# Optimization experiments

Measured on AMD Instinct MI355X. Metric: run time of the kernel, lower is better.

Reference implementation:

```python
import jax, jax.numpy as jnp
import numpy as np

N = 500_000
D = 256  # input_dim
H = 256  # hidden_dim
CLAMP = 10.0


def setup_inputs() -> dict:
    key = jax.random.key(0)
    ks = jax.random.split(key, 7)
    inputs = jax.random.normal(ks[0], (N, D), dtype=jnp.float32)
    query = jax.random.normal(ks[1], (D,), dtype=jnp.float32)
    mask = jax.random.randint(ks[2], (N,), 0, 2, dtype=jnp.int32)
    # nn.Linear(in, out, bias=False).weight has shape (out, in); scale like torch default
    s = 1.0 / np.sqrt(D)
    W_query = jax.random.uniform(ks[3], (H, D), jnp.float32, -s, s)
    W_key = jax.random.uniform(ks[4], (H, D), jnp.float32, -s, s)
    W_value = jax.random.uniform(ks[5], (H, D), jnp.float32, -s, s)
    sh = 1.0 / np.sqrt(H)
    W_out = jax.random.uniform(ks[6], (H,), jnp.float32, -sh, sh)
    return {"inputs": inputs, "query": query, "mask": mask,
            "W_query": W_query, "W_key": W_key, "W_value": W_value, "W_out": W_out}


def reference(inputs, query, mask, W_query, W_key, W_value, W_out):
    # Q: [H], K,V: [N,H]
    Q = W_query @ query
    K = jnp.einsum('nd,hd->nh', inputs, W_key)
    V = jnp.einsum('nd,hd->nh', inputs, W_value)
    scale = jnp.sqrt(jnp.asarray(H, dtype=inputs.dtype))
    scores = (K @ Q) / scale                      # [N]
    scores = jnp.where(mask == 0, -jnp.inf, scores)
    weights = jax.nn.softmax(scores, axis=-1)     # [N]
    attended = weights[:, None] * V               # [N,H] (elementwise, no sum)
    logits = attended @ W_out                     # [N]
    return CLAMP * jnp.tanh(logits)
```

## Files before the change

### kernel.cpp

```cpp
#include <hip/hip_runtime.h>
#include <math.h>

typedef float f4 __attribute__((ext_vector_type(4)));

#define DIM 256
#define NF4 64
#define NB_MAIN 2048

__device__ inline float dot4(f4 a, f4 b) {
  return a.x * b.x + a.y * b.y + a.z * b.z + a.w * b.w;
}

__device__ inline void sm_combine(float& m, float& l, float bm, float bl) {
  float mn = fmaxf(m, bm);
  float e1 = (l  != 0.f) ? __expf(m  - mn) : 0.f;
  float e2 = (bl != 0.f) ? __expf(bm - mn) : 0.f;
  l = l * e1 + bl * e2;
  m = mn;
}

__global__ void qba_compute_Q(const float* __restrict__ Wq,
                              const float* __restrict__ query,
                              float* __restrict__ Q) {
  int lane = threadIdx.x & 63;
  int wid  = threadIdx.x >> 6;
  int h = blockIdx.x * 4 + wid;
  f4 w = reinterpret_cast<const f4*>(Wq + (size_t)h * DIM)[lane];
  f4 q = reinterpret_cast<const f4*>(query)[lane];
  float acc = dot4(w, q);
  #pragma unroll
  for (int off = 32; off > 0; off >>= 1) acc += __shfl_xor(acc, off);
  if (lane == 0) Q[h] = acc;
}

__global__ void qba_compute_eff(const float* __restrict__ Wk,
                                const float* __restrict__ Wv,
                                const float* __restrict__ Q,
                                const float* __restrict__ Wout,
                                float* __restrict__ q_eff,
                                float* __restrict__ v_eff) {
  int d = threadIdx.x;
  if (blockIdx.x == 0) {
    float a = 0.f;
    #pragma unroll 8
    for (int h = 0; h < DIM; ++h) a += Wk[(size_t)h * DIM + d] * Q[h];
    q_eff[d] = a * 0.0625f;
  } else {
    float a = 0.f;
    #pragma unroll 8
    for (int h = 0; h < DIM; ++h) a += Wv[(size_t)h * DIM + d] * Wout[h];
    v_eff[d] = a;
  }
}

__global__ void __launch_bounds__(256)
qba_main(const float* __restrict__ inputs,
         const int* __restrict__ mask,
         const float* __restrict__ q_eff,
         const float* __restrict__ v_eff,
         float* __restrict__ s_buf,
         float* __restrict__ t_buf,
         float* __restrict__ block_m,
         float* __restrict__ block_l,
         int N) {
  int lane = threadIdx.x & 63;
  int wid  = threadIdx.x >> 6;
  int g    = lane >> 4;
  int sub  = lane & 15;
  const f4* in4 = reinterpret_cast<const f4*>(inputs);

  f4 qe[4], ve[4];
  #pragma unroll
  for (int k = 0; k < 4; ++k) {
    qe[k] = reinterpret_cast<const f4*>(q_eff)[sub + 16 * k];
    ve[k] = reinterpret_cast<const f4*>(v_eff)[sub + 16 * k];
  }

  int wave   = blockIdx.x * 4 + wid;
  int stride = NB_MAIN * 4 * 4;
  float m = -INFINITY, l = 0.f;

  for (int n0 = wave * 4; n0 < N; n0 += stride) {
    int row  = n0 + g;
    int rowc = row < N ? row : N - 1;
    const f4* rp = in4 + (size_t)rowc * NF4 + sub;
    f4 x0 = __builtin_nontemporal_load(rp);
    f4 x1 = __builtin_nontemporal_load(rp + 16);
    f4 x2 = __builtin_nontemporal_load(rp + 32);
    f4 x3 = __builtin_nontemporal_load(rp + 48);
    int mk = mask[rowc];

    float s = dot4(x0, qe[0]) + dot4(x1, qe[1]) + dot4(x2, qe[2]) + dot4(x3, qe[3]);
    float t = dot4(x0, ve[0]) + dot4(x1, ve[1]) + dot4(x2, ve[2]) + dot4(x3, ve[3]);
    #pragma unroll
    for (int off = 1; off < 16; off <<= 1) {
      s += __shfl_xor(s, off);
      t += __shfl_xor(t, off);
    }

    if (row < N) {
      if (sub == 0) {
        s_buf[row] = mk ? s : -INFINITY;
        t_buf[row] = t;
      }
      if (mk) {
        float mn = fmaxf(m, s);
        l = l * __expf(m - mn) + __expf(s - mn);
        m = mn;
      }
    }
  }

  #pragma unroll
  for (int off = 16; off < 64; off <<= 1) {
    float bm = __shfl_xor(m, off);
    float bl = __shfl_xor(l, off);
    sm_combine(m, l, bm, bl);
  }

  __shared__ float sm[4], sl[4];
  if (lane == 0) { sm[wid] = m; sl[wid] = l; }
  __syncthreads();
  if (threadIdx.x == 0) {
    float M = sm[0], L = sl[0];
    #pragma unroll
    for (int i = 1; i < 4; ++i) sm_combine(M, L, sm[i], sl[i]);
    block_m[blockIdx.x] = M;
    block_l[blockIdx.x] = L;
  }
}

__global__ void qba_combine(const float* __restrict__ block_m,
                            const float* __restrict__ block_l,
                            float* __restrict__ MS, int NB) {
  int tid = threadIdx.x;
  int lane = tid & 63, wid = tid >> 6;
  float m = -INFINITY, l = 0.f;
  for (int i = tid; i < NB; i += 256) sm_combine(m, l, block_m[i], block_l[i]);
  #pragma unroll
  for (int off = 32; off > 0; off >>= 1) {
    float bm = __shfl_xor(m, off);
    float bl = __shfl_xor(l, off);
    sm_combine(m, l, bm, bl);
  }
  __shared__ float sm[4], sl[4];
  if (lane == 0) { sm[wid] = m; sl[wid] = l; }
  __syncthreads();
  if (tid == 0) {
    float M = sm[0], L = sl[0];
    #pragma unroll
    for (int i = 1; i < 4; ++i) sm_combine(M, L, sm[i], sl[i]);
    MS[0] = M;
    MS[1] = 1.f / L;
  }
}

__global__ void qba_final(const f4* __restrict__ s4,
                          const f4* __restrict__ t4,
                          const float* __restrict__ MS,
                          f4* __restrict__ out4, int N4) {
  int i = blockIdx.x * blockDim.x + threadIdx.x;
  if (i >= N4) return;
  float M = MS[0], invS = MS[1];
  f4 s = s4[i], t = t4[i];
  f4 r;
  r.x = 10.f * tanhf(__expf(s.x - M) * invS * t.x);
  r.y = 10.f * tanhf(__expf(s.y - M) * invS * t.y);
  r.z = 10.f * tanhf(__expf(s.z - M) * invS * t.z);
  r.w = 10.f * tanhf(__expf(s.w - M) * invS * t.w);
  out4[i] = r;
}

extern "C" void kernel_launch(void* const* d_in, const int* in_sizes, int n_in,
                              void* d_out, int out_size, void* d_ws, size_t ws_size,
                              hipStream_t stream) {
  const float* inputs = (const float*)d_in[0];
  const float* query  = (const float*)d_in[1];
  const int*   mask   = (const int*)d_in[2];
  const float* Wq     = (const float*)d_in[3];
  const float* Wk     = (const float*)d_in[4];
  const float* Wv     = (const float*)d_in[5];
  const float* Wout   = (const float*)d_in[6];
  float* out = (float*)d_out;
  int N = in_sizes[2];

  float* ws     = (float*)d_ws;
  float* s_buf  = ws;
  float* t_buf  = s_buf + N;
  float* Qbuf   = t_buf + N;
  float* q_eff  = Qbuf + DIM;
  float* v_eff  = q_eff + DIM;
  float* bm     = v_eff + DIM;
  float* bl     = bm + NB_MAIN;
  float* MS     = bl + NB_MAIN;

  qba_compute_Q  <<<DIM / 4, 256, 0, stream>>>(Wq, query, Qbuf);
  qba_compute_eff<<<2, 256, 0, stream>>>(Wk, Wv, Qbuf, Wout, q_eff, v_eff);
  qba_main       <<<NB_MAIN, 256, 0, stream>>>(inputs, mask, q_eff, v_eff,
                                               s_buf, t_buf, bm, bl, N);
  qba_combine    <<<1, 256, 0, stream>>>(bm, bl, MS, NB_MAIN);
  qba_final      <<<(N / 4 + 255) / 256, 256, 0, stream>>>(
      (const f4*)s_buf, (const f4*)t_buf, MS, (f4*)out, N / 4);
}
```

Before: 102.9 us.

## Fuse softmax block-combine into main kernel via last-block atomic counter

The separate combine kernel is removed. Each block of the main kernel publishes its partial max and sum, then increments a global atomic counter, and the last block to arrive merges all partials and writes the normalizer. The weight-folding kernel now uses 1024 threads that split the hidden dimension four ways and reduce through shared memory. The main grid is halved to 1024 blocks and gets an occupancy hint. Together these cut one launch and shorten the serial setup kernel, at the cost of atomic traffic and fewer, longer-running blocks.

```diff
diff --git a/kernel.cpp b/kernel.cpp
--- a/kernel.cpp
+++ b/kernel.cpp
@@ -5,7 +5,7 @@
 
 #define DIM 256
 #define NF4 64
-#define NB_MAIN 2048
+#define NB_MAIN 1024
 
 __device__ inline float dot4(f4 a, f4 b) {
   return a.x * b.x + a.y * b.y + a.z * b.z + a.w * b.w;
@@ -21,7 +21,10 @@
 
 __global__ void qba_compute_Q(const float* __restrict__ Wq,
                               const float* __restrict__ query,
-                              float* __restrict__ Q) {
+                              float* __restrict__ Q,
+                              unsigned* __restrict__ counter) {
+  if (blockIdx.x == 0 && threadIdx.x == 0)
+    __hip_atomic_store(counter, 0u, __ATOMIC_RELAXED, __HIP_MEMORY_SCOPE_AGENT);
   int lane = threadIdx.x & 63;
   int wid  = threadIdx.x >> 6;
   int h = blockIdx.x * 4 + wid;
@@ -39,21 +42,28 @@
                                 const float* __restrict__ Wout,
                                 float* __restrict__ q_eff,
                                 float* __restrict__ v_eff) {
-  int d = threadIdx.x;
-  if (blockIdx.x == 0) {
-    float a = 0.f;
-    #pragma unroll 8
-    for (int h = 0; h < DIM; ++h) a += Wk[(size_t)h * DIM + d] * Q[h];
-    q_eff[d] = a * 0.0625f;
-  } else {
-    float a = 0.f;
-    #pragma unroll 8
-    for (int h = 0; h < DIM; ++h) a += Wv[(size_t)h * DIM + d] * Wout[h];
-    v_eff[d] = a;
-  }
-}
-
-__global__ void __launch_bounds__(256)
+  int tid = threadIdx.x;
+  int q = tid >> 8, d = tid & 255;
+  const float* W    = (blockIdx.x == 0) ? Wk : Wv;
+  const float* coef = (blockIdx.x == 0) ? Q  : Wout;
+  float a = 0.f;
+  int h0 = q * 64;
+  #pragma unroll 16
+  for (int i = 0; i < 64; ++i) {
+    int h = h0 + i;
+    a += W[(size_t)h * DIM + d] * coef[h];
+  }
+  __shared__ float part[4][DIM];
+  part[q][d] = a;
+  __syncthreads();
+  if (tid < DIM) {
+    float r = part[0][d] + part[1][d] + part[2][d] + part[3][d];
+    if (blockIdx.x == 0) q_eff[d] = r * 0.0625f;
+    else                 v_eff[d] = r;
+  }
+}
+
+__global__ void __launch_bounds__(256, 4)
 qba_main(const float* __restrict__ inputs,
          const int* __restrict__ mask,
          const float* __restrict__ q_eff,
@@ -62,6 +72,8 @@
          float* __restrict__ t_buf,
          float* __restrict__ block_m,
          float* __restrict__ block_l,
+         float* __restrict__ MS,
+         unsigned* __restrict__ counter,
          int N) {
   int lane = threadIdx.x & 63;
   int wid  = threadIdx.x >> 6;
@@ -77,7 +89,7 @@
   }
 
   int wave   = blockIdx.x * 4 + wid;
-  int stride = NB_MAIN * 4 * 4;
+  const int stride = NB_MAIN * 16;
   float m = -INFINITY, l = 0.f;
 
   for (int n0 = wave * 4; n0 < N; n0 += stride) {
@@ -119,39 +131,45 @@
   }
 
   __shared__ float sm[4], sl[4];
+  __shared__ bool amLast;
   if (lane == 0) { sm[wid] = m; sl[wid] = l; }
   __syncthreads();
   if (threadIdx.x == 0) {
     float M = sm[0], L = sl[0];
     #pragma unroll
     for (int i = 1; i < 4; ++i) sm_combine(M, L, sm[i], sl[i]);
-    block_m[blockIdx.x] = M;
-    block_l[blockIdx.x] = L;
-  }
-}
-
-__global__ void qba_combine(const float* __restrict__ block_m,
-                            const float* __restrict__ block_l,
-                            float* __restrict__ MS, int NB) {
-  int tid = threadIdx.x;
-  int lane = tid & 63, wid = tid >> 6;
-  float m = -INFINITY, l = 0.f;
-  for (int i = tid; i < NB; i += 256) sm_combine(m, l, block_m[i], block_l[i]);
-  #pragma unroll
-  for (int off = 32; off > 0; off >>= 1) {
-    float bm = __shfl_xor(m, off);
-    float bl = __shfl_xor(l, off);
-    sm_combine(m, l, bm, bl);
-  }
-  __shared__ float sm[4], sl[4];
-  if (lane == 0) { sm[wid] = m; sl[wid] = l; }
+    __hip_atomic_store(&block_m[blockIdx.x], M, __ATOMIC_RELEASE, __HIP_MEMORY_SCOPE_AGENT);
+    __hip_atomic_store(&block_l[blockIdx.x], L, __ATOMIC_RELEASE, __HIP_MEMORY_SCOPE_AGENT);
+    unsigned prev = __hip_atomic_fetch_add(counter, 1u, __ATOMIC_ACQ_REL, __HIP_MEMORY_SCOPE_AGENT);
+    amLast = (prev == (unsigned)(gridDim.x - 1));
+  }
   __syncthreads();
-  if (tid == 0) {
-    float M = sm[0], L = sl[0];
+
+  if (amLast) {
+    int tid = threadIdx.x;
+    float cm = -INFINITY, cl = 0.f;
+    for (int i = tid; i < NB_MAIN; i += 256) {
+      float bm = __hip_atomic_load(&block_m[i], __ATOMIC_ACQUIRE, __HIP_MEMORY_SCOPE_AGENT);
+      float bl = __hip_atomic_load(&block_l[i], __ATOMIC_ACQUIRE, __HIP_MEMORY_SCOPE_AGENT);
+      sm_combine(cm, cl, bm, bl);
+    }
     #pragma unroll
-    for (int i = 1; i < 4; ++i) sm_combine(M, L, sm[i], sl[i]);
-    MS[0] = M;
-    MS[1] = 1.f / L;
+    for (int off = 32; off > 0; off >>= 1) {
+      float bm = __shfl_xor(cm, off);
+      float bl = __shfl_xor(cl, off);
+      sm_combine(cm, cl, bm, bl);
+    }
+    __syncthreads();
+    if (lane == 0) { sm[wid] = cm; sl[wid] = cl; }
+    __syncthreads();
+    if (tid == 0) {
+      float M = sm[0], L = sl[0];
+      #pragma unroll
+      for (int i = 1; i < 4; ++i) sm_combine(M, L, sm[i], sl[i]);
+      MS[0] = M;
+      MS[1] = 1.f / L;
+      __hip_atomic_store(counter, 0u, __ATOMIC_RELEASE, __HIP_MEMORY_SCOPE_AGENT);
+    }
   }
 }
 
@@ -193,12 +211,12 @@
   float* bm     = v_eff + DIM;
   float* bl     = bm + NB_MAIN;
   float* MS     = bl + NB_MAIN;
-
-  qba_compute_Q  <<<DIM / 4, 256, 0, stream>>>(Wq, query, Qbuf);
-  qba_compute_eff<<<2, 256, 0, stream>>>(Wk, Wv, Qbuf, Wout, q_eff, v_eff);
+  unsigned* cnt = (unsigned*)(MS + 2);
+
+  qba_compute_Q  <<<DIM / 4, 256, 0, stream>>>(Wq, query, Qbuf, cnt);
+  qba_compute_eff<<<2, 1024, 0, stream>>>(Wk, Wv, Qbuf, Wout, q_eff, v_eff);
   qba_main       <<<NB_MAIN, 256, 0, stream>>>(inputs, mask, q_eff, v_eff,
-                                               s_buf, t_buf, bm, bl, N);
-  qba_combine    <<<1, 256, 0, stream>>>(bm, bl, MS, NB_MAIN);
+                                               s_buf, t_buf, bm, bl, MS, cnt, N);
   qba_final      <<<(N / 4 + 255) / 256, 256, 0, stream>>>(
       (const f4*)s_buf, (const f4*)t_buf, MS, (f4*)out, N / 4);
 }
```

Measured after the change: 187.7 us. 82.4% more time.

## Fuse prep kernels and combine into final pass, interleave score/value buffers

Applied to the files above, without the earlier changes.

Merges the Q projection and effective-weight kernels into one 1024-thread prep kernel that splits the reduction over h into four partial sums. Folds the global softmax combine into every block of the final kernel, so each block redundantly reduces the 2048 block partials instead of running a separate single-block launch. Stores score and value as interleaved float2 pairs in one buffer. The aim is fewer kernel launches and serial tiny stages, at the cost of redundant combine work in each final block.

```diff
diff --git a/kernel.cpp b/kernel.cpp
--- a/kernel.cpp
+++ b/kernel.cpp
@@ -2,6 +2,7 @@
 #include <math.h>
 
 typedef float f4 __attribute__((ext_vector_type(4)));
+typedef float f2 __attribute__((ext_vector_type(2)));
 
 #define DIM 256
 #define NF4 64
@@ -19,37 +20,51 @@
   m = mn;
 }
 
-__global__ void qba_compute_Q(const float* __restrict__ Wq,
-                              const float* __restrict__ query,
-                              float* __restrict__ Q) {
-  int lane = threadIdx.x & 63;
-  int wid  = threadIdx.x >> 6;
-  int h = blockIdx.x * 4 + wid;
-  f4 w = reinterpret_cast<const f4*>(Wq + (size_t)h * DIM)[lane];
-  f4 q = reinterpret_cast<const f4*>(query)[lane];
-  float acc = dot4(w, q);
-  #pragma unroll
-  for (int off = 32; off > 0; off >>= 1) acc += __shfl_xor(acc, off);
-  if (lane == 0) Q[h] = acc;
-}
-
-__global__ void qba_compute_eff(const float* __restrict__ Wk,
-                                const float* __restrict__ Wv,
-                                const float* __restrict__ Q,
-                                const float* __restrict__ Wout,
-                                float* __restrict__ q_eff,
-                                float* __restrict__ v_eff) {
-  int d = threadIdx.x;
+__global__ void qba_prep(const float* __restrict__ Wq,
+                         const float* __restrict__ query,
+                         const float* __restrict__ Wk,
+                         const float* __restrict__ Wv,
+                         const float* __restrict__ Wout,
+                         float* __restrict__ q_eff,
+                         float* __restrict__ v_eff) {
+  __shared__ float Qs[DIM];
+  __shared__ float part[4][DIM];
+  int tid = threadIdx.x;
+  int q = tid >> 8, d = tid & 255;
   if (blockIdx.x == 0) {
+    int lane = tid & 63, w = tid >> 6;
+    f4 qv = reinterpret_cast<const f4*>(query)[lane];
+    #pragma unroll 4
+    for (int i = 0; i < 16; ++i) {
+      int h = w * 16 + i;
+      f4 wv = reinterpret_cast<const f4*>(Wq + (size_t)h * DIM)[lane];
+      float acc = dot4(wv, qv);
+      #pragma unroll
+      for (int off = 32; off > 0; off >>= 1) acc += __shfl_xor(acc, off);
+      if (lane == 0) Qs[h] = acc;
+    }
+    __syncthreads();
     float a = 0.f;
-    #pragma unroll 8
-    for (int h = 0; h < DIM; ++h) a += Wk[(size_t)h * DIM + d] * Q[h];
-    q_eff[d] = a * 0.0625f;
+    #pragma unroll 16
+    for (int i = 0; i < 64; ++i) {
+      int h = q * 64 + i;
+      a += Wk[(size_t)h * DIM + d] * Qs[h];
+    }
+    part[q][d] = a;
+    __syncthreads();
+    if (tid < DIM)
+      q_eff[tid] = (part[0][tid] + part[1][tid] + part[2][tid] + part[3][tid]) * 0.0625f;
   } else {
     float a = 0.f;
-    #pragma unroll 8
-    for (int h = 0; h < DIM; ++h) a += Wv[(size_t)h * DIM + d] * Wout[h];
-    v_eff[d] = a;
+    #pragma unroll 16
+    for (int i = 0; i < 64; ++i) {
+      int h = q * 64 + i;
+      a += Wv[(size_t)h * DIM + d] * Wout[h];
+    }
+    part[q][d] = a;
+    __syncthreads();
+    if (tid < DIM)
+      v_eff[tid] = part[0][tid] + part[1][tid] + part[2][tid] + part[3][tid];
   }
 }
 
@@ -58,8 +73,7 @@
          const int* __restrict__ mask,
          const float* __restrict__ q_eff,
          const float* __restrict__ v_eff,
-         float* __restrict__ s_buf,
-         float* __restrict__ t_buf,
+         f2* __restrict__ st_buf,
          float* __restrict__ block_m,
          float* __restrict__ block_l,
          int N) {
@@ -77,7 +91,7 @@
   }
 
   int wave   = blockIdx.x * 4 + wid;
-  int stride = NB_MAIN * 4 * 4;
+  const int stride = NB_MAIN * 16;
   float m = -INFINITY, l = 0.f;
 
   for (int n0 = wave * 4; n0 < N; n0 += stride) {
@@ -100,8 +114,8 @@
 
     if (row < N) {
       if (sub == 0) {
-        s_buf[row] = mk ? s : -INFINITY;
-        t_buf[row] = t;
+        f2 v; v.x = mk ? s : -INFINITY; v.y = t;
+        st_buf[row] = v;
       }
       if (mk) {
         float mn = fmaxf(m, s);
@@ -130,13 +144,20 @@
   }
 }
 
-__global__ void qba_combine(const float* __restrict__ block_m,
-                            const float* __restrict__ block_l,
-                            float* __restrict__ MS, int NB) {
+__global__ void __launch_bounds__(256)
+qba_final(const f2* __restrict__ st,
+          const float* __restrict__ block_m,
+          const float* __restrict__ block_l,
+          f4* __restrict__ out4, int N4) {
   int tid = threadIdx.x;
   int lane = tid & 63, wid = tid >> 6;
+
   float m = -INFINITY, l = 0.f;
-  for (int i = tid; i < NB; i += 256) sm_combine(m, l, block_m[i], block_l[i]);
+  #pragma unroll
+  for (int k = 0; k < NB_MAIN / 256; ++k) {
+    int i = tid + k * 256;
+    sm_combine(m, l, block_m[i], block_l[i]);
+  }
   #pragma unroll
   for (int off = 32; off > 0; off >>= 1) {
     float bm = __shfl_xor(m, off);
@@ -144,30 +165,29 @@
     sm_combine(m, l, bm, bl);
   }
   __shared__ float sm[4], sl[4];
+  __shared__ float MSs[2];
   if (lane == 0) { sm[wid] = m; sl[wid] = l; }
   __syncthreads();
   if (tid == 0) {
     float M = sm[0], L = sl[0];
     #pragma unroll
     for (int i = 1; i < 4; ++i) sm_combine(M, L, sm[i], sl[i]);
-    MS[0] = M;
-    MS[1] = 1.f / L;
-  }
-}
-
-__global__ void qba_final(const f4* __restrict__ s4,
-                          const f4* __restrict__ t4,
-                          const float* __restrict__ MS,
-                          f4* __restrict__ out4, int N4) {
-  int i = blockIdx.x * blockDim.x + threadIdx.x;
+    MSs[0] = M;
+    MSs[1] = 1.f / L;
+  }
+  __syncthreads();
+
+  int i = blockIdx.x * 256 + tid;
   if (i >= N4) return;
-  float M = MS[0], invS = MS[1];
-  f4 s = s4[i], t = t4[i];
+  float M = MSs[0], invS = MSs[1];
+  const f4* st4 = reinterpret_cast<const f4*>(st);
+  f4 a = st4[2 * i];
+  f4 b = st4[2 * i + 1];
   f4 r;
-  r.x = 10.f * tanhf(__expf(s.x - M) * invS * t.x);
-  r.y = 10.f * tanhf(__expf(s.y - M) * invS * t.y);
-  r.z = 10.f * tanhf(__expf(s.z - M) * invS * t.z);
-  r.w = 10.f * tanhf(__expf(s.w - M) * invS * t.w);
+  r.x = 10.f * tanhf(__expf(a.x - M) * invS * a.y);
+  r.y = 10.f * tanhf(__expf(a.z - M) * invS * a.w);
+  r.z = 10.f * tanhf(__expf(b.x - M) * invS * b.y);
+  r.w = 10.f * tanhf(__expf(b.z - M) * invS * b.w);
   out4[i] = r;
 }
 
@@ -185,20 +205,15 @@
   int N = in_sizes[2];
 
   float* ws     = (float*)d_ws;
-  float* s_buf  = ws;
-  float* t_buf  = s_buf + N;
-  float* Qbuf   = t_buf + N;
-  float* q_eff  = Qbuf + DIM;
+  f2*    st_buf = (f2*)ws;
+  float* q_eff  = ws + 2 * N;
   float* v_eff  = q_eff + DIM;
   float* bm     = v_eff + DIM;
   float* bl     = bm + NB_MAIN;
-  float* MS     = bl + NB_MAIN;
-
-  qba_compute_Q  <<<DIM / 4, 256, 0, stream>>>(Wq, query, Qbuf);
-  qba_compute_eff<<<2, 256, 0, stream>>>(Wk, Wv, Qbuf, Wout, q_eff, v_eff);
-  qba_main       <<<NB_MAIN, 256, 0, stream>>>(inputs, mask, q_eff, v_eff,
-                                               s_buf, t_buf, bm, bl, N);
-  qba_combine    <<<1, 256, 0, stream>>>(bm, bl, MS, NB_MAIN);
-  qba_final      <<<(N / 4 + 255) / 256, 256, 0, stream>>>(
-      (const f4*)s_buf, (const f4*)t_buf, MS, (f4*)out, N / 4);
-}
+
+  qba_prep <<<2, 1024, 0, stream>>>(Wq, query, Wk, Wv, Wout, q_eff, v_eff);
+  qba_main <<<NB_MAIN, 256, 0, stream>>>(inputs, mask, q_eff, v_eff,
+                                         st_buf, bm, bl, N);
+  qba_final<<<(N / 4 + 255) / 256, 256, 0, stream>>>(
+      st_buf, bm, bl, (f4*)out, N / 4);
+}
```

Result: faster. 93.94 us (-8.7%).
